# Performance work log

Measured on AMD Instinct MI355X. Metric: run time of the kernel, lower is better.

The kernel has to match this reference:

```python
import jax, jax.numpy as jnp
import numpy as np

B, N, A = 2, 4096, 5
TOPK = 30
K_RBF = 16
MAX_AA = 22
MAXREL = 32
EDGE_IN = 16 + K_RBF * 25 + 14 + 16  # 446
EDGE_FEAT = 128
PI = 3.1415926


def l2norm(v, eps=1e-12):
    n = jnp.sqrt(jnp.sum(v * v, axis=-1, keepdims=True))
    return v / jnp.maximum(n, eps)


def gather_nodes(nodes, idx):
    # nodes: (B,N,C), idx: (B,N,K) -> (B,N,K,C)
    b, n, k = idx.shape
    flat = idx.reshape(b, n * k, 1)
    out = jnp.take_along_axis(nodes, flat, axis=1)
    return out.reshape(b, n, k, nodes.shape[-1])


def quaternions(R):
    # R: (...,3,3) -> unit quaternion (...,4)
    Rxx, Ryy, Rzz = R[..., 0, 0], R[..., 1, 1], R[..., 2, 2]
    mag = 0.5 * jnp.sqrt(jnp.abs(1.0 + jnp.stack([Rxx - Ryy - Rzz, -Rxx + Ryy - Rzz, -Rxx - Ryy + Rzz], -1)) + 1e-12)
    signs = jnp.sign(jnp.stack([R[..., 2, 1] - R[..., 1, 2], R[..., 0, 2] - R[..., 2, 0], R[..., 1, 0] - R[..., 0, 1]], -1))
    xyz = signs * mag
    w = jnp.sqrt(jax.nn.relu(1.0 + Rxx + Ryy + Rzz) + 1e-12)[..., None] / 2.0
    return l2norm(jnp.concatenate([xyz, w], -1))


def setup_inputs():
    key = jax.random.key(0)
    ks = jax.random.split(key, 12)
    X = jax.random.normal(ks[0], (B, N, A, 3), jnp.float32) * 3.0
    mask = jnp.ones((B, N), jnp.float32)
    mask_atoms = jnp.ones((B, N, A), jnp.float32)
    means = jax.random.normal(ks[1], (K_RBF,), jnp.float32)
    stds = jax.random.normal(ks[2], (K_RBF,), jnp.float32)
    mul_w = jax.random.normal(ks[3], (A * A,), jnp.float32)
    bias_w = jax.random.normal(ks[4], (A * A,), jnp.float32)
    aa_pair_embed = jax.random.normal(ks[5], (MAX_AA * MAX_AA, K_RBF), jnp.float32) * 0.02
    aa_pair_embed = aa_pair_embed.at[441].set(0.0)  # padding_idx
    relpos_embed = jax.random.normal(ks[6], (2 * MAXREL + 1, 16), jnp.float32) * 0.02
    mask_embed = jax.random.normal(ks[7], (2, 16), jnp.float32) * 0.02
    W1 = jax.random.normal(ks[8], (EDGE_IN, EDGE_IN), jnp.float32) / np.sqrt(EDGE_IN)
    b1 = jnp.zeros((EDGE_IN,), jnp.float32)
    W2 = jax.random.normal(ks[9], (EDGE_IN, EDGE_FEAT), jnp.float32) / np.sqrt(EDGE_IN)
    b2 = jnp.zeros((EDGE_FEAT,), jnp.float32)
    aa = jax.random.randint(ks[10], (B, N), 0, 21, jnp.int32)
    residue_idx = jnp.tile(jnp.arange(N, dtype=jnp.int32)[None, :], (B, 1))
    chain_labels = jax.random.randint(ks[11], (B, N), 0, 2, jnp.int32)
    return dict(X=X, mask=mask, mask_atoms=mask_atoms, means=means, stds=stds, mul_w=mul_w,
                bias_w=bias_w, aa_pair_embed=aa_pair_embed, relpos_embed=relpos_embed,
                mask_embed=mask_embed, W1=W1, b1=b1, W2=W2, b2=b2, aa=aa,
                residue_idx=residue_idx, chain_labels=chain_labels)


def reference(X, mask, mask_atoms, means, stds, mul_w, bias_w, aa_pair_embed, relpos_embed,
              mask_embed, W1, b1, W2, b2, aa, residue_idx, chain_labels):
    Ca = X[:, :, 1]  # (B,N,3) C-alpha
    # ---- _dist: spatial kNN over C-alpha ----
    mask2d = mask[:, :, None] * mask[:, None, :]
    dx = Ca[:, None, :, :] - Ca[:, :, None, :]
    D = mask2d * jnp.sqrt(jnp.sum(dx * dx, -1) + 1e-6)
    D_adj = D + (1.0 - mask2d) * jnp.max(D, -1, keepdims=True)
    _, E_idx = jax.lax.top_k(-D_adj, TOPK)  # smallest distances
    mask_attend = jnp.take_along_axis(mask2d, E_idx, axis=2)  # (B,N,K)
    # ---- orientation features (local frames + quaternions) ----
    ones3 = jnp.ones((B, 1, 3), X.dtype)
    u = l2norm(jnp.concatenate([ones3, Ca[:, 1:] - Ca[:, :-1]], 1))
    b_ = l2norm(jnp.concatenate([u[:, :-1] - u[:, 1:], ones3], 1))
    n_ = l2norm(jnp.concatenate([jnp.cross(u[:, :-1], u[:, 1:]), ones3], 1))
    lf = jnp.stack([b_, n_, jnp.cross(b_, n_)], axis=2)  # (B,N,3,3)
    X_nb = gather_nodes(Ca, E_idx)                       # (B,N,K,3)
    O_nb = gather_nodes(lf.reshape(B, N, 9), E_idx).reshape(B, N, TOPK, 3, 3)
    t = X_nb - Ca[:, :, None, :]
    t = jnp.einsum('bnij,bnkj->bnki', lf, t)
    t = l2norm(t) * mask_attend[..., None]
    r = jnp.einsum('bnji,bnkjl->bnkil', lf, O_nb)  # lf^T @ O_nb
    q = quaternions(r) * mask_attend[..., None]
    O_feat = jnp.concatenate([t, q, 1.0 - 2.0 * jnp.abs(t), 1.0 - 2.0 * jnp.abs(q)], -1)  # (B,N,K,14)
    # ---- positional / chain embeddings ----
    offset = residue_idx[:, :, None] - residue_idx[:, None, :]
    offset_nb = jnp.take_along_axis(offset, E_idx, 2)
    d_chain = (chain_labels[:, :, None] == chain_labels[:, None, :]).astype(jnp.int32)
    E_chains = jnp.take_along_axis(d_chain, E_idx, 2)
    d = jnp.clip(offset_nb + MAXREL, 0, 2 * MAXREL)
    E_pos = relpos_embed[d] + mask_embed[E_chains]  # (B,N,K,16)
    # ---- GaussianLayer: aa-pair embed + atom-pair distance RBF ----
    aa_pair = aa[:, :, None] * MAX_AA + aa[:, None, :]
    aa_nb = jnp.take_along_axis(aa_pair, E_idx, 2)
    feat_aapair = aa_pair_embed[aa_nb] * mask_attend[..., None]  # (B,N,K,16)
    nbX = gather_nodes(X.reshape(B, N, A * 3), E_idx).reshape(B, N, TOPK, A, 3)
    delta = nbX[:, :, :, :, None, :] - X[:, :, None, None, :, :]  # (B,N,K,A,A,3)
    Dab = jnp.sqrt(jnp.sum(delta * delta, -1) + 1e-12)            # (B,N,K,A,A)
    et = jnp.arange(A * A).reshape(A, A)
    xg = mul_w[et] * Dab + bias_w[et]
    m_nb = gather_nodes(mask_atoms, E_idx)  # (B,N,K,A)
    xg = xg * (m_nb[..., None, :] * m_nb[..., :, None])
    std = jnp.abs(stds) + 0.01
    g = jnp.exp(-0.5 * ((xg[..., None] - means) / std) ** 2) / ((2.0 * PI) ** 0.5 * std)
    gbf = g.reshape(B, N, TOPK, A * A * K_RBF) * mask_attend[..., None]  # (B,N,K,400)
    # ---- fuse and project (NonLinear gbf_proj) ----
    E = jnp.concatenate([E_pos, gbf, O_feat, feat_aapair], -1)  # (B,N,K,446)
    h = jax.nn.gelu(E @ W1 + b1, approximate=False)
    return h @ W2 + b2  # (B,N,K,128)
```

## Files before the change

kernel.cpp:

```cpp
#include <hip/hip_runtime.h>
#include <cstdint>
#include <cstddef>

#define NN 4096
#define TOPK_ 30
#define BN_TOT 8192
#define M_TOT 245760
#define KP 448
#define HSTRIDE 136
#define EF 128

typedef unsigned short u16;
typedef unsigned int u32;
typedef __attribute__((ext_vector_type(8))) short bf16x8;
typedef __attribute__((ext_vector_type(4))) float f32x4;

__device__ __forceinline__ float b2f(u16 u){ return __uint_as_float(((u32)u)<<16); }
__device__ __forceinline__ u16 f2b(float f){
  u32 u = __float_as_uint(f);
  return (u16)((u + 0x7FFFu + ((u>>16)&1u)) >> 16);
}
__device__ __forceinline__ float ldf(const void* p, long i, int fl){
  return fl ? ((const float*)p)[i] : b2f(((const u16*)p)[i]);
}
__device__ __forceinline__ int is_f32_flag(const u16* mask){
  return (((const u32*)mask)[0] == 0x3F800000u) ? 1 : 0;
}
__device__ __forceinline__ void norm3(float x,float y,float z,float&ox,float&oy,float&oz){
  float n = sqrtf(x*x+y*y+z*z); n = fmaxf(n, 1e-12f);
  ox=x/n; oy=y/n; oz=z/n;
}
__device__ __forceinline__ float sgn(float x){ return x>0.f?1.f:(x<0.f?-1.f:0.f); }
__device__ __forceinline__ float gelu_f(float x){
  return 0.5f*x*(1.0f + erff(x*0.70710678118654752440f));
}
__device__ __forceinline__ void async_cp16(const void* g, void* l){
  __builtin_amdgcn_global_load_lds((const __attribute__((address_space(1))) void*)(uintptr_t)g,
                                   (__attribute__((address_space(3))) void*)(uintptr_t)l, 16, 0, 0);
}

__global__ __launch_bounds__(256) void prep_kernel(
    const void* __restrict__ X, const u16* __restrict__ mask,
    const void* __restrict__ W1, const void* __restrict__ b1,
    const void* __restrict__ W2, const void* __restrict__ b2,
    float* __restrict__ ca, float* __restrict__ lf,
    u16* __restrict__ W1P, u16* __restrict__ W2P,
    float* __restrict__ b1p, float* __restrict__ b2p)
{
  const int fl = is_f32_flag(mask);
  int idx = blockIdx.x*256 + threadIdx.x;
  if (idx < BN_TOT) {
    int i = idx & (NN-1);
    float cax = ldf(X, (long)idx*15+3, fl), cay = ldf(X, (long)idx*15+4, fl), caz = ldf(X, (long)idx*15+5, fl);
    ca[idx*4+0]=cax; ca[idx*4+1]=cay; ca[idx*4+2]=caz; ca[idx*4+3]=0.f;
    float bx,by,bz,nx,ny,nz;
    if (i < NN-1) {
      float uix,uiy,uiz;
      if (i==0) { norm3(1.f,1.f,1.f,uix,uiy,uiz); }
      else {
        float px=ldf(X,(long)(idx-1)*15+3,fl), py=ldf(X,(long)(idx-1)*15+4,fl), pz=ldf(X,(long)(idx-1)*15+5,fl);
        norm3(cax-px, cay-py, caz-pz, uix,uiy,uiz);
      }
      float qx=ldf(X,(long)(idx+1)*15+3,fl), qy=ldf(X,(long)(idx+1)*15+4,fl), qz=ldf(X,(long)(idx+1)*15+5,fl);
      float vx,vy,vz; norm3(qx-cax, qy-cay, qz-caz, vx,vy,vz);
      norm3(uix-vx, uiy-vy, uiz-vz, bx,by,bz);
      norm3(uiy*vz-uiz*vy, uiz*vx-uix*vz, uix*vy-uiy*vx, nx,ny,nz);
    } else {
      norm3(1.f,1.f,1.f,bx,by,bz); nx=bx; ny=by; nz=bz;
    }
    float cx = by*nz - bz*ny, cy = bz*nx - bx*nz, cz = bx*ny - by*nx;
    float* L = lf + (size_t)idx*12;
    L[0]=bx;L[1]=by;L[2]=bz;L[3]=nx;L[4]=ny;L[5]=nz;L[6]=cx;L[7]=cy;L[8]=cz;
    return;
  }
  int r1 = idx - BN_TOT;
  if (r1 < 229376) {
    int f = r1 >> 9, li = r1 & 511;
    int n0 = f / 14, kc = f - n0*14;
    int ln = li >> 3, j = li & 7;
    int n = n0*16 + (ln & 15);
    int k = kc*32 + (ln >> 4)*8 + j;
    W1P[r1] = (n < 446 && k < 446) ? (fl ? f2b(((const float*)W1)[(long)k*446 + n])
                                         : ((const u16*)W1)[(long)k*446 + n]) : (u16)0;
    return;
  }
  int r2 = r1 - 229376;
  if (r2 < 65536) {
    int f = r2 >> 9, li = r2 & 511;
    int n0 = f >> 4, kc = f & 15;
    int ln = li >> 3, j = li & 7;
    int n = n0*16 + (ln & 15);
    int k = kc*32 + (ln >> 4)*8 + j;
    W2P[r2] = (k < 446) ? (fl ? f2b(((const float*)W2)[(long)k*128 + n])
                              : ((const u16*)W2)[(long)k*128 + n]) : (u16)0;
    return;
  }
  int r3 = r2 - 65536;
  if (r3 < 512) { b1p[r3] = (r3<446)? ldf(b1, r3, fl) : 0.f; return; }
  int r4 = r3 - 512;
  if (r4 < 128) { b2p[r4] = ldf(b2, r4, fl); }
}

__global__ __launch_bounds__(64) void knn_kernel(const float4* __restrict__ ca,
                                                 int* __restrict__ eidx)
{
#pragma clang fp contract(off)
  __shared__ u32 keys[NN];
  int bi = blockIdx.x;
  int lane = threadIdx.x;
  int b = bi >> 12;
  const float4 ci = ca[bi];
  const float4* cab = ca + (b<<12);
  u32 mind = 0xFFFFFFFFu; int minj = 1<<30; int minslot = 0;
  for (int c = 0; c < 64; ++c) {
    int j = (c<<6) | lane;
    float4 cj = cab[j];
    float dx = cj.x-ci.x, dy = cj.y-ci.y, dz = cj.z-ci.z;
    float ss = dx*dx;
    ss = ss + dy*dy;
    ss = ss + dz*dz;
    float d = sqrtf(ss + 1e-6f);
    u32 db = __float_as_uint(d);
    keys[(c<<6)|lane] = db;
    if (db < mind) { mind = db; minj = j; minslot = c; }
  }
  __syncthreads();
  for (int r = 0; r < TOPK_; ++r) {
    u32 wd = mind; int wj = minj;
    #pragma unroll
    for (int off = 32; off; off >>= 1) {
      u32 od = __shfl_xor(wd, off, 64);
      int oj = __shfl_xor(wj, off, 64);
      if (od < wd || (od == wd && oj < wj)) { wd = od; wj = oj; }
    }
    if (lane == 0) eidx[bi*TOPK_ + r] = wj;
    if ((wj & 63) == lane && wj == minj) {
      keys[minslot*64 + lane] = 0xFFFFFFFFu;
      mind = 0xFFFFFFFFu; minj = 1<<30;
      for (int c = 0; c < 64; ++c) {
        u32 db = keys[(c<<6)|lane];
        if (db < mind) { mind = db; minj = (c<<6)|lane; minslot = c; }
      }
    }
  }
}

__global__ __launch_bounds__(256) void ofeat_kernel(
  const u16* __restrict__ mask, const float* __restrict__ ca, const float* __restrict__ lf,
  const int* __restrict__ eidx, u16* __restrict__ E, int chunkStart, int Mc)
{
  int t = blockIdx.x*256 + threadIdx.x;
  if (t >= Mc) return;
  long e = chunkStart + t;
  const int fl = is_f32_flag(mask);
  int k = (int)(e % TOPK_);
  long bi = e / TOPK_;
  int b = (int)(bi >> 12);
  int bj = (b<<12) + eidx[bi*TOPK_ + k];
  float ma = ldf(mask, bi, fl) * ldf(mask, bj, fl);
  float Li[9], Lj[9];
  #pragma unroll
  for (int q_ = 0; q_ < 9; ++q_) { Li[q_] = lf[(size_t)bi*12+q_]; Lj[q_] = lf[(size_t)bj*12+q_]; }
  float dx = ca[bj*4+0]-ca[bi*4+0], dy = ca[bj*4+1]-ca[bi*4+1], dz = ca[bj*4+2]-ca[bi*4+2];
  float t0 = Li[0]*dx+Li[1]*dy+Li[2]*dz;
  float t1 = Li[3]*dx+Li[4]*dy+Li[5]*dz;
  float t2 = Li[6]*dx+Li[7]*dy+Li[8]*dz;
  float tn = fmaxf(sqrtf(t0*t0+t1*t1+t2*t2), 1e-12f);
  t0 = t0/tn*ma; t1 = t1/tn*ma; t2 = t2/tn*ma;
  float R00=Li[0]*Lj[0]+Li[3]*Lj[3]+Li[6]*Lj[6];
  float R01=Li[0]*Lj[1]+Li[3]*Lj[4]+Li[6]*Lj[7];
  float R02=Li[0]*Lj[2]+Li[3]*Lj[5]+Li[6]*Lj[8];
  float R10=Li[1]*Lj[0]+Li[4]*Lj[3]+Li[7]*Lj[6];
  float R11=Li[1]*Lj[1]+Li[4]*Lj[4]+Li[7]*Lj[7];
  float R12=Li[1]*Lj[2]+Li[4]*Lj[5]+Li[7]*Lj[8];
  float R20=Li[2]*Lj[0]+Li[5]*Lj[3]+Li[8]*Lj[6];
  float R21=Li[2]*Lj[1]+Li[5]*Lj[4]+Li[8]*Lj[7];
  float R22=Li[2]*Lj[2]+Li[5]*Lj[5]+Li[8]*Lj[8];
  float m0 = 0.5f*sqrtf(fabsf(1.f+R00-R11-R22)+1e-12f);
  float m1 = 0.5f*sqrtf(fabsf(1.f-R00+R11-R22)+1e-12f);
  float m2 = 0.5f*sqrtf(fabsf(1.f-R00-R11+R22)+1e-12f);
  float q0 = sgn(R21-R12)*m0, q1 = sgn(R02-R20)*m1, q2 = sgn(R10-R01)*m2;
  float qw = 0.5f*sqrtf(fmaxf(1.f+R00+R11+R22, 0.f)+1e-12f);
  float qn = fmaxf(sqrtf(q0*q0+q1*q1+q2*q2+qw*qw), 1e-12f);
  q0 = q0/qn*ma; q1 = q1/qn*ma; q2 = q2/qn*ma; qw = qw/qn*ma;
  u16 vals[14];
  vals[0]=f2b(t0); vals[1]=f2b(t1); vals[2]=f2b(t2);
  vals[3]=f2b(q0); vals[4]=f2b(q1); vals[5]=f2b(q2); vals[6]=f2b(qw);
  vals[7]=f2b(1.f-2.f*fabsf(t0)); vals[8]=f2b(1.f-2.f*fabsf(t1)); vals[9]=f2b(1.f-2.f*fabsf(t2));
  vals[10]=f2b(1.f-2.f*fabsf(q0)); vals[11]=f2b(1.f-2.f*fabsf(q1));
  vals[12]=f2b(1.f-2.f*fabsf(q2)); vals[13]=f2b(1.f-2.f*fabsf(qw));
  u16* dst = E + (size_t)t*KP + 416;
  *(uint4*)dst = *(const uint4*)vals;
  *(uint2*)(dst+8) = *(const uint2*)(vals+8);
  *(u32*)(dst+12) = *(const u32*)(vals+12);
}

__global__ __launch_bounds__(256) void feat_kernel(
  const void* __restrict__ X, const u16* __restrict__ mask, const void* __restrict__ mask_atoms,
  const void* __restrict__ means, const void* __restrict__ stds,
  const void* __restrict__ mul_w, const void* __restrict__ bias_w,
  const void* __restrict__ aa_pe, const void* __restrict__ relpos, const void* __restrict__ mask_emb,
  const int* __restrict__ aa, const int* __restrict__ ridx, const int* __restrict__ chains,
  const int* __restrict__ eidx, u16* __restrict__ E, int chunkStart, int Mc)
{
  const int fl = is_f32_flag(mask);
  int lane = threadIdx.x & 63;
  long gw = (long)(blockIdx.x*4) + (threadIdx.x >> 6);
  long nw = (long)gridDim.x * 4;
  float stdv = fabsf(ldf(stds, lane & 15, fl)) + 0.01f;
  float rinv = 1.0f/stdv;
  float coef0 = 0.3989422804014327f*rinv;
  float rmean = ldf(means, lane & 15, fl);
  float mw = 0.f, bw = 0.f;
  if (lane < 25) { mw = ldf(mul_w, lane, fl); bw = ldf(bias_w, lane, fl); }
  for (long e = chunkStart + gw; e < chunkStart + Mc; e += nw) {
    int k = (int)(e % TOPK_);
    long bi = e / TOPK_;
    int b = (int)(bi >> 12);
    int bj = (b<<12) + eidx[bi*TOPK_ + k];
    float ma = ldf(mask, bi, fl) * ldf(mask, bj, fl);
    float xgv = 0.f;
    if (lane < 25) {
      int a = lane/5, c_ = lane - a*5;
      float d0 = ldf(X,(long)bj*15 + a*3+0,fl) - ldf(X,(long)bi*15 + c_*3+0,fl);
      float d1 = ldf(X,(long)bj*15 + a*3+1,fl) - ldf(X,(long)bi*15 + c_*3+1,fl);
      float d2 = ldf(X,(long)bj*15 + a*3+2,fl) - ldf(X,(long)bi*15 + c_*3+2,fl);
      float Dab = sqrtf(d0*d0 + d1*d1 + d2*d2 + 1e-12f);
      float mm = ldf(mask_atoms,(long)bj*5 + a,fl) * ldf(mask_atoms,(long)bj*5 + c_,fl);
      xgv = (mw*Dab + bw) * mm;
    }
    int d = ridx[bi] - ridx[bj] + 32; d = d < 0 ? 0 : (d > 64 ? 64 : d);
    int ch = (chains[bi] == chains[bj]) ? 1 : 0;
    int aap = aa[bi]*22 + aa[bj];
    u16* row = E + (size_t)(e - chunkStart) * KP;
    #pragma unroll
    for (int pass = 0; pass < 7; ++pass) {
      int f = pass*64 + lane;
      int p = (f - 16) >> 4;
      p = p < 0 ? 0 : (p > 24 ? 24 : p);
      float xv = __shfl(xgv, p, 64);
      float val; bool skip = false;
      if (f < 16) {
        val = ldf(relpos, d*16 + f, fl) + ldf(mask_emb, ch*16 + f, fl);
      } else if (f < 416) {
        float z = (xv - rmean) * rinv;
        val = __expf(-0.5f*z*z) * coef0 * ma;
      } else if (f < 430) {
        skip = true; val = 0.f;
      } else if (f < 446) {
        val = ldf(aa_pe, aap*16 + (f-430), fl) * ma;
      } else {
        val = 0.f;
      }
      if (!skip) row[f] = f2b(val);
    }
  }
}

__global__ __launch_bounds__(512,2) void fused_mlp(
    const u16* __restrict__ E, const u16* __restrict__ W1P, const u16* __restrict__ W2P,
    const float* __restrict__ b1p, const float* __restrict__ b2p,
    void* __restrict__ C, long outOff, const u16* maskp)
{
  __shared__ u16 smem[128*HSTRIDE];
  u16* hs = smem;
  int tid = threadIdx.x;
  int lane = tid & 63, wave = tid >> 6;
  int wr = wave >> 2, wc = wave & 3;
  long rowBase = (long)blockIdx.x * 128;

  #define STAGE(tt, buf) do {                                                     \
    int r0_ = tid >> 3, s0_ = tid & 7;                                            \
    async_cp16(E + (rowBase + r0_)*(long)KP + (tt)*64 + ((s0_ ^ (r0_ & 7))<<3),   \
               smem + (buf)*8192 + tid*8);                                        \
    int r1_ = 64 + r0_;                                                           \
    async_cp16(E + (rowBase + r1_)*(long)KP + (tt)*64 + ((s0_ ^ (r1_ & 7))<<3),   \
               smem + (buf)*8192 + 4096 + tid*8);                                 \
  } while(0)

  f32x4 acc1[4][4][2] = {};
  STAGE(0, 0);
  #pragma unroll 1
  for (int t = 0; t < 7; ++t) {
    __syncthreads();
    const u16* As = smem + (t&1)*8192;
    bf16x8 af[2][4];
    #pragma unroll
    for (int kk = 0; kk < 2; ++kk)
      #pragma unroll
      for (int r = 0; r < 4; ++r) {
        int row = wr*64 + r*16 + (lane&15);
        int s = kk*4 + (lane>>4);
        af[kk][r] = *(const bf16x8*)(As + row*64 + ((s ^ (row&7))<<3));
      }
    bf16x8 bgA[2][2][2];
    #pragma unroll
    for (int c = 0; c < 2; ++c)
      #pragma unroll
      for (int cc = 0; cc < 2; ++cc)
        #pragma unroll
        for (int kk = 0; kk < 2; ++kk)
          bgA[c][cc][kk] = *(const bf16x8*)(W1P + (((c*8 + wc*2 + cc)*14 + t*2 + kk) << 9) + lane*8);
    __builtin_amdgcn_sched_barrier(0);
    if (t < 6) STAGE(t+1, (t+1)&1);
    #pragma unroll
    for (int c = 0; c < 2; ++c)
      #pragma unroll
      for (int r = 0; r < 4; ++r)
        #pragma unroll
        for (int cc = 0; cc < 2; ++cc)
          #pragma unroll
          for (int kk = 0; kk < 2; ++kk)
            acc1[c][r][cc] = __builtin_amdgcn_mfma_f32_16x16x32_bf16(af[kk][r], bgA[c][cc][kk], acc1[c][r][cc], 0,0,0);
    bf16x8 bgB[2][2][2];
    #pragma unroll
    for (int c = 0; c < 2; ++c)
      #pragma unroll
      for (int cc = 0; cc < 2; ++cc)
        #pragma unroll
        for (int kk = 0; kk < 2; ++kk)
          bgB[c][cc][kk] = *(const bf16x8*)(W1P + ((((c+2)*8 + wc*2 + cc)*14 + t*2 + kk) << 9) + lane*8);
    #pragma unroll
    for (int c = 0; c < 2; ++c)
      #pragma unroll
      for (int r = 0; r < 4; ++r)
        #pragma unroll
        for (int cc = 0; cc < 2; ++cc)
          #pragma unroll
          for (int kk = 0; kk < 2; ++kk)
            acc1[c+2][r][cc] = __builtin_amdgcn_mfma_f32_16x16x32_bf16(af[kk][r], bgB[c][cc][kk], acc1[c+2][r][cc], 0,0,0);
  }
  #undef STAGE

  f32x4 acc2[4][2] = {};
  #pragma unroll
  for (int c = 0; c < 4; ++c) {
    __syncthreads();
    #pragma unroll
    for (int r = 0; r < 4; ++r)
      #pragma unroll
      for (int cc = 0; cc < 2; ++cc) {
        int col = wc*32 + cc*16 + (lane & 15);
        float bv = b1p[c*128 + col];
        #pragma unroll
        for (int g = 0; g < 4; ++g) {
          int row = wr*64 + r*16 + (lane>>4)*4 + g;
          hs[row*HSTRIDE + col] = f2b(gelu_f(acc1[c][r][cc][g] + bv));
        }
      }
    __syncthreads();
    #pragma unroll
    for (int k2 = 0; k2 < 4; ++k2) {
      bf16x8 af2[4], bg2[2];
      #pragma unroll
      for (int r = 0; r < 4; ++r) {
        int row = wr*64 + r*16 + (lane&15);
        af2[r] = *(const bf16x8*)(hs + row*HSTRIDE + k2*32 + (lane>>4)*8);
      }
      #pragma unroll
      for (int cc = 0; cc < 2; ++cc)
        bg2[cc] = *(const bf16x8*)(W2P + ((((wc*2+cc)*16) + c*4 + k2) << 9) + lane*8);
      #pragma unroll
      for (int r = 0; r < 4; ++r)
        #pragma unroll
        for (int cc = 0; cc < 2; ++cc)
          acc2[r][cc] = __builtin_amdgcn_mfma_f32_16x16x32_bf16(af2[r], bg2[cc], acc2[r][cc], 0,0,0);
    }
  }

  const int f32out = is_f32_flag(maskp);
  #pragma unroll
  for (int r = 0; r < 4; ++r) {
    #pragma unroll
    for (int cc = 0; cc < 2; ++cc) {
      int col = wc*32 + cc*16 + (lane & 15);
      float bv = b2p[col];
      #pragma unroll
      for (int g = 0; g < 4; ++g) {
        long row = rowBase + wr*64 + r*16 + (lane>>4)*4 + g;
        float v = acc2[r][cc][g] + bv;
        long o = outOff + row*EF + col;
        if (f32out) ((float*)C)[o] = v;
        else        ((u16*)C)[o]  = f2b(v);
      }
    }
  }
}

extern "C" void kernel_launch(void* const* d_in, const int* in_sizes, int n_in,
                              void* d_out, int out_size, void* d_ws, size_t ws_size,
                              hipStream_t stream) {
  const void* X          = d_in[0];
  const u16* mask        = (const u16*)d_in[1];
  const void* mask_atoms = d_in[2];
  const void* means      = d_in[3];
  const void* stds       = d_in[4];
  const void* mul_w      = d_in[5];
  const void* bias_w     = d_in[6];
  const void* aa_pe      = d_in[7];
  const void* relpos     = d_in[8];
  const void* mask_emb   = d_in[9];
  const void* W1         = d_in[10];
  const void* b1         = d_in[11];
  const void* W2         = d_in[12];
  const void* b2         = d_in[13];
  const int* aa          = (const int*)d_in[14];
  const int* ridx        = (const int*)d_in[15];
  const int* chains      = (const int*)d_in[16];

  char* ws = (char*)d_ws;
  float* ca  = (float*)(ws + 0);
  float* lf  = (float*)(ws + 131072);
  int* eidx  = (int*)(ws + 524288);
  u16* W1P   = (u16*)(ws + 1507328);
  u16* W2P   = (u16*)(ws + 1966080);
  float* b1p = (float*)(ws + 2097152);
  float* b2p = (float*)(ws + 2099200);
  size_t base = 2099712;

  int nc = 64;
  for (int c = 1; c <= 64; c <<= 1) {
    size_t mc = (size_t)M_TOT / c;
    if (base + mc*896 <= ws_size) { nc = c; break; }
  }
  int Mc = M_TOT / nc;
  u16* Ebuf = (u16*)(ws + base);

  prep_kernel<<<1187, 256, 0, stream>>>(X, mask, W1, b1, W2, b2, ca, lf, W1P, W2P, b1p, b2p);
  knn_kernel<<<BN_TOT, 64, 0, stream>>>((const float4*)ca, eidx);
  for (int c = 0; c < nc; ++c) {
    int cs = c * Mc;
    feat_kernel<<<1024, 256, 0, stream>>>(X, mask, mask_atoms, means, stds, mul_w, bias_w,
                                          aa_pe, relpos, mask_emb, aa, ridx, chains,
                                          eidx, Ebuf, cs, Mc);
    ofeat_kernel<<<Mc/256, 256, 0, stream>>>(mask, ca, lf, eidx, Ebuf, cs, Mc);
    fused_mlp<<<Mc/128, 512, 0, stream>>>(Ebuf, W1P, W2P, b1p, b2p, d_out,
                                          (long)cs*EF, mask);
  }
}
```

Baseline: 804.6 us.

## Double-buffer hidden tile, use fast erf GELU, and move async staging later

The second-GEMM phase gets a double-buffered LDS hidden tile, so the GELU of the next 128-column chunk is written while MFMAs consume the current one, halving the barriers per chunk. The exact erff GELU is replaced with the Abramowitz-Stegun polynomial erf plus a packed bf16 conversion instruction. The async prefetch of the next E tile is moved after the second weight-fragment load and fenced with sched barriers. Shared memory per block doubles, which could limit the occupancy of two blocks per CU, and the erf approximation adds small numerical error.

```diff
diff --git a/kernel.cpp b/kernel.cpp
--- a/kernel.cpp
+++ b/kernel.cpp
@@ -33,6 +33,23 @@
 __device__ __forceinline__ float sgn(float x){ return x>0.f?1.f:(x<0.f?-1.f:0.f); }
 __device__ __forceinline__ float gelu_f(float x){
   return 0.5f*x*(1.0f + erff(x*0.70710678118654752440f));
+}
+__device__ __forceinline__ float gelu_fast(float x){
+  float y = 0.70710678118654752440f * x;
+  float s = fabsf(y);
+  float t = __builtin_amdgcn_rcpf(fmaf(0.3275911f, s, 1.0f));
+  float p = fmaf(fmaf(fmaf(fmaf(1.061405429f, t, -1.453152027f), t, 1.421413741f), t,
+                 -0.284496736f), t, 0.254829592f);
+  float e = __expf(-y*y);
+  float erfs = fmaf(-p*t, e, 1.0f);
+  float erfy = (x >= 0.f) ? erfs : -erfs;
+  float hx = 0.5f*x;
+  return fmaf(hx, erfy, hx);
+}
+__device__ __forceinline__ u32 pk_bf16(float lo, float hi){
+  u32 r;
+  asm("v_cvt_pk_bf16_f32 %0, %1, %2" : "=v"(r) : "v"(lo), "v"(hi));
+  return r;
 }
 __device__ __forceinline__ void async_cp16(const void* g, void* l){
   __builtin_amdgcn_global_load_lds((const __attribute__((address_space(1))) void*)(uintptr_t)g,
@@ -262,8 +279,9 @@
     const float* __restrict__ b1p, const float* __restrict__ b2p,
     void* __restrict__ C, long outOff, const u16* maskp)
 {
-  __shared__ u16 smem[128*HSTRIDE];
-  u16* hs = smem;
+  __shared__ u16 smem[2*128*HSTRIDE];
+  u16* hs0 = smem;
+  u16* hs1 = smem + 128*HSTRIDE;
   int tid = threadIdx.x;
   int lane = tid & 63, wave = tid >> 6;
   int wr = wave >> 2, wc = wave & 3;
@@ -301,8 +319,6 @@
         #pragma unroll
         for (int kk = 0; kk < 2; ++kk)
           bgA[c][cc][kk] = *(const bf16x8*)(W1P + (((c*8 + wc*2 + cc)*14 + t*2 + kk) << 9) + lane*8);
-    __builtin_amdgcn_sched_barrier(0);
-    if (t < 6) STAGE(t+1, (t+1)&1);
     #pragma unroll
     for (int c = 0; c < 2; ++c)
       #pragma unroll
@@ -320,6 +336,9 @@
         #pragma unroll
         for (int kk = 0; kk < 2; ++kk)
           bgB[c][cc][kk] = *(const bf16x8*)(W1P + ((((c+2)*8 + wc*2 + cc)*14 + t*2 + kk) << 9) + lane*8);
+    __builtin_amdgcn_sched_barrier(0);
+    if (t < 6) STAGE(t+1, (t+1)&1);
+    __builtin_amdgcn_sched_barrier(0);
     #pragma unroll
     for (int c = 0; c < 2; ++c)
       #pragma unroll
@@ -332,30 +351,41 @@
   }
   #undef STAGE
 
+  #define STORE_HS(cN, buf) do {                                                  \
+    _Pragma("unroll")                                                             \
+    for (int r = 0; r < 4; ++r) {                                                 \
+      _Pragma("unroll")                                                           \
+      for (int cc = 0; cc < 2; ++cc) {                                            \
+        int col = wc*32 + cc*16 + (lane & 15);                                    \
+        float bv = b1p[(cN)*128 + col];                                           \
+        int row0 = wr*64 + r*16 + (lane>>4)*4;                                    \
+        u32 p01 = pk_bf16(gelu_fast(acc1[cN][r][cc][0]+bv),                       \
+                          gelu_fast(acc1[cN][r][cc][1]+bv));                      \
+        u32 p23 = pk_bf16(gelu_fast(acc1[cN][r][cc][2]+bv),                       \
+                          gelu_fast(acc1[cN][r][cc][3]+bv));                      \
+        u16* hb_ = (buf) + row0*HSTRIDE + col;                                    \
+        hb_[0]         = (u16)p01; hb_[HSTRIDE]   = (u16)(p01>>16);               \
+        hb_[2*HSTRIDE] = (u16)p23; hb_[3*HSTRIDE] = (u16)(p23>>16);               \
+      }                                                                           \
+    }                                                                             \
+  } while(0)
+
   f32x4 acc2[4][2] = {};
+  __syncthreads();
+  STORE_HS(0, hs0);
+  __syncthreads();
   #pragma unroll
   for (int c = 0; c < 4; ++c) {
-    __syncthreads();
-    #pragma unroll
-    for (int r = 0; r < 4; ++r)
-      #pragma unroll
-      for (int cc = 0; cc < 2; ++cc) {
-        int col = wc*32 + cc*16 + (lane & 15);
-        float bv = b1p[c*128 + col];
-        #pragma unroll
-        for (int g = 0; g < 4; ++g) {
-          int row = wr*64 + r*16 + (lane>>4)*4 + g;
-          hs[row*HSTRIDE + col] = f2b(gelu_f(acc1[c][r][cc][g] + bv));
-        }
-      }
-    __syncthreads();
+    u16* hb = (c & 1) ? hs1 : hs0;
+    u16* hn = (c & 1) ? hs0 : hs1;
+    if (c < 3) STORE_HS(c+1, hn);
     #pragma unroll
     for (int k2 = 0; k2 < 4; ++k2) {
       bf16x8 af2[4], bg2[2];
       #pragma unroll
       for (int r = 0; r < 4; ++r) {
         int row = wr*64 + r*16 + (lane&15);
-        af2[r] = *(const bf16x8*)(hs + row*HSTRIDE + k2*32 + (lane>>4)*8);
+        af2[r] = *(const bf16x8*)(hb + row*HSTRIDE + k2*32 + (lane>>4)*8);
       }
       #pragma unroll
       for (int cc = 0; cc < 2; ++cc)
@@ -366,7 +396,9 @@
         for (int cc = 0; cc < 2; ++cc)
           acc2[r][cc] = __builtin_amdgcn_mfma_f32_16x16x32_bf16(af2[r], bg2[cc], acc2[r][cc], 0,0,0);
     }
-  }
+    __syncthreads();
+  }
+  #undef STORE_HS
 
   const int f32out = is_f32_flag(maskp);
   #pragma unroll
```

Measured after the change: 785.1 us. -2.4%, faster.
